# Kernel optimization log

Measured on AMD Instinct MI355X. Metric: run time of the kernel, lower is better.

The kernel has to match this reference:

```python
import jax, jax.numpy as jnp
import numpy as np

N = 20000      # nodes
E = 640000     # edges
HID = 128      # hidden_dim
HEADS = 8
HD = HID // HEADS  # head_dim = 16


def setup_inputs() -> dict:
    key = jax.random.key(0)
    ks = jax.random.split(key, 32)
    s = 1.0 / np.sqrt(HID)
    d = {}
    d["h"] = jax.random.normal(ks[0], (N, HID), jnp.float32)
    d["x"] = jax.random.normal(ks[1], (N, 3), jnp.float32)
    d["src"] = jax.random.randint(ks[2], (E,), 0, N)
    d["dst"] = jax.random.randint(ks[3], (E,), 0, N)
    d["distances"] = jax.random.uniform(ks[4], (E,), jnp.float32)
    d["bpp_edge_bias"] = jax.random.uniform(ks[5], (E,), jnp.float32)
    d["msa_edge_bias"] = jax.random.uniform(ks[6], (E,), jnp.float32)
    d["chem_edge_bias"] = jax.random.uniform(ks[7], (E,), jnp.float32)
    d["relative_offset"] = jax.random.normal(ks[8], (E,), jnp.float32)
    d["chain_break_mask"] = jax.random.uniform(ks[9], (E,), jnp.float32)
    # attention projections (nn.Linear(hidden, hidden): y = x @ W + b)
    for i, nm in enumerate(["Wq", "Wk", "Wv", "Wo"]):
        d[nm] = jax.random.normal(ks[10 + i], (HID, HID), jnp.float32) * s
    for nm in ["bq", "bk", "bv", "bo"]:
        d[nm] = jnp.zeros((HID,), jnp.float32)
    # six Linear(1, heads) edge-bias heads -> weight vector [HEADS] + bias [HEADS]
    for i, nm in enumerate(["dist", "bpp", "msa", "chem", "rel", "chain"]):
        d["w_" + nm] = jax.random.normal(ks[14 + i], (HEADS,), jnp.float32) * 0.1
        d["b_" + nm] = jnp.zeros((HEADS,), jnp.float32)
    # coord_gate: Linear(HID,HID) -> SiLU -> Linear(HID,1) -> Tanh
    d["Wg1"] = jax.random.normal(ks[20], (HID, HID), jnp.float32) * s
    d["bg1"] = jnp.zeros((HID,), jnp.float32)
    d["wg2"] = jax.random.normal(ks[21], (HID, 1), jnp.float32) * s
    d["bg2"] = jnp.zeros((1,), jnp.float32)
    return d


def _edge_bias(feat, w, b):
    # Linear(1, heads) applied to per-edge scalar: [E] -> [E, HEADS]
    return feat[:, None] * w[None, :] + b[None, :]


def reference(h, x, src, dst, distances, bpp_edge_bias, msa_edge_bias,
              chem_edge_bias, relative_offset, chain_break_mask,
              Wq, bq, Wk, bk, Wv, bv, Wo, bo,
              w_dist, b_dist, w_bpp, b_bpp, w_msa, b_msa,
              w_chem, b_chem, w_rel, b_rel, w_chain, b_chain,
              Wg1, bg1, wg2, bg2):
    n = h.shape[0]
    q = (h @ Wq + bq).reshape(n, HEADS, HD)
    k = (h @ Wk + bk).reshape(n, HEADS, HD)
    v = (h @ Wv + bv).reshape(n, HEADS, HD)
    q_src = q[src]   # [E, H, D]
    k_dst = k[dst]
    v_dst = v[dst]
    logits = jnp.einsum('ehd,ehd->eh', q_src, k_dst) / np.sqrt(float(HD))
    logits = (logits
              - _edge_bias(distances * distances, w_dist, b_dist)
              + _edge_bias(bpp_edge_bias, w_bpp, b_bpp)
              + _edge_bias(msa_edge_bias, w_msa, b_msa)
              + _edge_bias(chem_edge_bias, w_chem, b_chem)
              + _edge_bias(relative_offset, w_rel, b_rel)
              + _edge_bias(chain_break_mask, w_chain, b_chain))
    # segment softmax over edges grouped by src node, per head
    m = jax.ops.segment_max(logits, src, num_segments=n)        # [N, H]
    ex = jnp.exp(logits - m[src])                               # [E, H]
    denom = jax.ops.segment_sum(ex, src, num_segments=n)        # [N, H]
    weights = ex / jnp.maximum(denom[src], 1e-9)                # [E, H]
    # weighted scatter-aggregate of values to src nodes
    h_update = jax.ops.segment_sum(v_dst * weights[:, :, None], src,
                                   num_segments=n).reshape(n, HID)
    h_out = h + h_update @ Wo + bo
    # coordinate update
    weights_mean = weights.mean(axis=1)                         # [E]
    disp = jax.ops.segment_sum((x[dst] - x[src]) * weights_mean[:, None],
                               src, num_segments=n)             # [N, 3]
    gate = jnp.tanh(jax.nn.silu(h_out @ Wg1 + bg1) @ wg2 + bg2)  # [N, 1]
    x_out = x + gate * disp
    return h_out, x_out
```

## Files before the change

### kernel.cpp

```cpp
#include <hip/hip_runtime.h>
#include <hip/hip_bf16.h>

#define N_NODES 20000
#define N_EDGES 640000
#define HID 128
#define HEADS 8
#define HD 16
#define NB_SCAN ((N_NODES + 255) / 256)
#define CH 160
#define QKV_BLOCKS 625
#define PREP_BLOCKS 5

typedef __attribute__((ext_vector_type(8))) short bf16x8;
typedef __attribute__((ext_vector_type(4))) float f32x4;

__device__ __forceinline__ float bflo(unsigned u) {
    union { unsigned i; float f; } x; x.i = u << 16; return x.f;
}
__device__ __forceinline__ float bfhi(unsigned u) {
    union { unsigned i; float f; } x; x.i = u & 0xffff0000u; return x.f;
}
__device__ __forceinline__ float bfu(ushort u) {
    union { unsigned i; float f; } x; x.i = ((unsigned)u) << 16; return x.f;
}
__device__ __forceinline__ ushort f2bu(float f) {
    __hip_bfloat16 b = __float2bfloat16(f);
    union { __hip_bfloat16 b; ushort u; } c; c.b = b; return c.u;
}

__global__ __launch_bounds__(256) void hist_prep_kernel(const int* __restrict__ src,
        int* __restrict__ cnt, int* __restrict__ rank,
        const float* __restrict__ Wq, const float* __restrict__ Wk,
        const float* __restrict__ Wv, const float* __restrict__ Wo,
        const float* __restrict__ Wg1, ushort* __restrict__ Wt) {
    if (blockIdx.x < PREP_BLOCKS) {
        const float* srcs[5] = {Wq, Wk, Wv, Wo, Wg1};
        const float* W = srcs[blockIdx.x];
        ushort* out = Wt + (size_t)blockIdx.x * 16384;
        for (int i = threadIdx.x; i < 16384; i += 256) {
            int k = i >> 7, n = i & 127;
            out[n * 128 + k] = f2bu(W[i]);
        }
    } else {
        const int e = (blockIdx.x - PREP_BLOCKS) * 256 + threadIdx.x;
        rank[e] = atomicAdd(&cnt[src[e]], 1);
    }
}

__global__ __launch_bounds__(256) void scan1_kernel(const int* __restrict__ cnt,
        int* __restrict__ startp, int* __restrict__ blockSums, int n) {
    __shared__ int sd[256];
    const int tid = threadIdx.x;
    const int i = blockIdx.x * 256 + tid;
    int xv = (i < n) ? cnt[i] : 0;
    sd[tid] = xv;
    __syncthreads();
#pragma unroll
    for (int off = 1; off < 256; off <<= 1) {
        int tv = (tid >= off) ? sd[tid - off] : 0;
        __syncthreads();
        sd[tid] += tv;
        __syncthreads();
    }
    if (i < n) startp[i] = sd[tid] - xv;
    if (tid == 255) blockSums[blockIdx.x] = sd[255];
}

__global__ __launch_bounds__(128) void scan2_kernel(int* __restrict__ blockSums, int nb) {
    __shared__ int sd[128];
    const int tid = threadIdx.x;
    int xv = (tid < nb) ? blockSums[tid] : 0;
    sd[tid] = xv;
    __syncthreads();
#pragma unroll
    for (int off = 1; off < 128; off <<= 1) {
        int tv = (tid >= off) ? sd[tid - off] : 0;
        __syncthreads();
        sd[tid] += tv;
        __syncthreads();
    }
    if (tid < nb) blockSums[tid] = sd[tid] - xv;
    if (tid == 127) blockSums[nb] = sd[127];
}

__global__ __launch_bounds__(256) void scatter_qkv_kernel(
        const float* __restrict__ h, const ushort* __restrict__ Wt,
        const float* __restrict__ bq, const float* __restrict__ bk,
        const float* __restrict__ bv,
        ushort* __restrict__ qb, ushort* __restrict__ kb, ushort* __restrict__ vb,
        const int* __restrict__ src, const int* __restrict__ dst,
        const float* __restrict__ dist, const float* __restrict__ bpp,
        const float* __restrict__ msa, const float* __restrict__ chem,
        const float* __restrict__ rel, const float* __restrict__ chain,
        const float* __restrict__ w_dist, const float* __restrict__ b_dist,
        const float* __restrict__ w_bpp, const float* __restrict__ b_bpp,
        const float* __restrict__ w_msa, const float* __restrict__ b_msa,
        const float* __restrict__ w_chem, const float* __restrict__ b_chem,
        const float* __restrict__ w_rel, const float* __restrict__ b_rel,
        const float* __restrict__ w_chain, const float* __restrict__ b_chain,
        const int* __restrict__ startp, const int* __restrict__ blockSums,
        const int* __restrict__ rank, const float* __restrict__ x,
        uint4* __restrict__ recs) {
    __shared__ __align__(16) ushort hs[32 * 136];
    const int t = threadIdx.x;
    if (blockIdx.x < QKV_BLOCKS) {
        const int row0 = blockIdx.x * 32;
        for (int i = t; i < 4096; i += 256)
            hs[(i >> 7) * 136 + (i & 127)] = f2bu(h[(size_t)row0 * 128 + i]);
        __syncthreads();
        const int w = t >> 6, lane = t & 63;
        const int rt = w >> 1, half = w & 1;
        const int lrow = lane & 15, lkb = (lane >> 4) * 8;
        bf16x8 a[4];
#pragma unroll
        for (int ks = 0; ks < 4; ++ks)
            a[ks] = *reinterpret_cast<const bf16x8*>(&hs[(rt * 16 + lrow) * 136 + ks * 32 + lkb]);
        __syncthreads();
        const int rloc0 = rt * 16 + (lane >> 4) * 4;
#define DO_MAT(MI, BIAS, OUT) \
        { \
        for (int ctp = 0; ctp < 4; ++ctp) { \
            const int col = (ctp * 2 + half) * 16 + lrow; \
            f32x4 acc = {0.f, 0.f, 0.f, 0.f}; \
            _Pragma("unroll") \
            for (int ks = 0; ks < 4; ++ks) { \
                bf16x8 b = *reinterpret_cast<const bf16x8*>( \
                    &Wt[MI * 16384 + col * 128 + ks * 32 + lkb]); \
                acc = __builtin_amdgcn_mfma_f32_16x16x32_bf16(a[ks], b, acc, 0, 0, 0); \
            } \
            const float bias = BIAS[col]; \
            _Pragma("unroll") \
            for (int r = 0; r < 4; ++r) \
                hs[(rloc0 + r) * 128 + col] = f2bu(acc[r] + bias); \
        } \
        __syncthreads(); \
        { \
            uint4* outp = reinterpret_cast<uint4*>(OUT + (size_t)row0 * 128); \
            const uint4* inp = reinterpret_cast<const uint4*>(hs); \
            outp[t] = inp[t]; \
            outp[t + 256] = inp[t + 256]; \
        } \
        __syncthreads(); \
        }
        DO_MAT(0, bq, qb)
        DO_MAT(1, bk, kb)
        DO_MAT(2, bv, vb)
#undef DO_MAT
    } else {
        const int e = (blockIdx.x - QKV_BLOCKS) * 256 + t;
        const int s = src[e];
        const int pos = startp[s] + blockSums[s >> 8] + rank[e];
        const int dn = dst[e];
        const float d2 = dist[e] * dist[e];
        const float f_bpp = bpp[e], f_msa = msa[e], f_chem = chem[e];
        const float f_rel = rel[e], f_chain = chain[e];
        ushort o16[8];
#pragma unroll
        for (int hq = 0; hq < 8; ++hq) {
            float b = -(d2 * w_dist[hq] + b_dist[hq])
                    + (f_bpp * w_bpp[hq] + b_bpp[hq])
                    + (f_msa * w_msa[hq] + b_msa[hq])
                    + (f_chem * w_chem[hq] + b_chem[hq])
                    + (f_rel * w_rel[hq] + b_rel[hq])
                    + (f_chain * w_chain[hq] + b_chain[hq]);
            o16[hq] = f2bu(b);
        }
        uint4 rec0;
        rec0.x = (unsigned)o16[0] | ((unsigned)o16[1] << 16);
        rec0.y = (unsigned)o16[2] | ((unsigned)o16[3] << 16);
        rec0.z = (unsigned)o16[4] | ((unsigned)o16[5] << 16);
        rec0.w = (unsigned)o16[6] | ((unsigned)o16[7] << 16);
        const float* xp = &x[(size_t)dn * 3];
        uint4 rec1;
        rec1.x = (unsigned)dn;
        rec1.y = __float_as_uint(xp[0]);
        rec1.z = __float_as_uint(xp[1]);
        rec1.w = __float_as_uint(xp[2]);
        recs[(size_t)pos * 2]     = rec0;
        recs[(size_t)pos * 2 + 1] = rec1;
    }
}

__global__ __launch_bounds__(256) void node_kernel(const ushort* __restrict__ qb,
        const ushort* __restrict__ kb, const ushort* __restrict__ vb,
        const uint4* __restrict__ recs, const float* __restrict__ x,
        const int* __restrict__ startp, const int* __restrict__ blockSums,
        ushort* __restrict__ hub, float* __restrict__ disp) {
    __shared__ float qLds[4 * 128];
    __shared__ float xsLds[12];
    __shared__ int   sLds[5];
    __shared__ int   dnLds[CH];
    __shared__ float xLds[CH * 3];
    __shared__ __align__(16) ushort biasLds[CH * 8];
    __shared__ float peLds[CH * 8];
    __shared__ float redN[4][32][9];

    const int t = threadIdx.x;
    const int n0 = blockIdx.x * 4;

    if (t < 64) {
        uint4 qv = reinterpret_cast<const uint4*>(qb + (size_t)n0 * 128)[t];
        const unsigned* qu = reinterpret_cast<const unsigned*>(&qv);
        float4 f0 = make_float4(bflo(qu[0]), bfhi(qu[0]), bflo(qu[1]), bfhi(qu[1]));
        float4 f1 = make_float4(bflo(qu[2]), bfhi(qu[2]), bflo(qu[3]), bfhi(qu[3]));
        *reinterpret_cast<float4*>(&qLds[t * 8])     = f0;
        *reinterpret_cast<float4*>(&qLds[t * 8 + 4]) = f1;
    }
    if (t < 12) xsLds[t] = x[(size_t)n0 * 3 + t];
    if (t < 5) {
        int idx = n0 + t;
        sLds[t] = (idx < N_NODES) ? (startp[idx] + blockSums[idx >> 8]) : N_EDGES;
    }
    __syncthreads();

    const int S0 = sLds[0], S4 = sLds[4];
    const int s1r = sLds[1], s2r = sLds[2], s3r = sLds[3];

    const int eg = t >> 5;
    const int dq = t & 31;
    const int hh = dq >> 2;
    const int jj = dq & 3;
    const int j3 = (jj < 3) ? jj : 0;

    float acc0[4] = {0,0,0,0}, acc1[4] = {0,0,0,0};
    float acc2[4] = {0,0,0,0}, acc3[4] = {0,0,0,0};
    float den0 = 0, den1 = 0, den2 = 0, den3 = 0;
    float adx0 = 0, adx1 = 0, adx2 = 0, adx3 = 0;

    for (int base = S0; base < S4; base += CH) {
        const int en = min(CH, S4 - base);
        __syncthreads();
        if (t < en) {
            const uint4 r0 = recs[(size_t)(base + t) * 2];
            const uint4 r1 = recs[(size_t)(base + t) * 2 + 1];
            *reinterpret_cast<uint4*>(&biasLds[t * 8]) = r0;
            dnLds[t] = (int)r1.x;
            xLds[t * 3 + 0] = __uint_as_float(r1.y);
            xLds[t * 3 + 1] = __uint_as_float(r1.z);
            xLds[t * 3 + 2] = __uint_as_float(r1.w);
        }
        __syncthreads();
        const int np = en * 8;
#define PA_BODY(P) { \
            const int e = (P) >> 3, ha = (P) & 7; \
            const int ge = base + e; \
            const int m = (ge >= s1r) + (ge >= s2r) + (ge >= s3r); \
            const ushort* krow = kb + (size_t)dnLds[e] * 128 + ha * 16; \
            const uint4 ka = *reinterpret_cast<const uint4*>(krow); \
            const uint4 kb4 = *reinterpret_cast<const uint4*>(krow + 8); \
            const float* qrow = &qLds[m * 128 + ha * 16]; \
            const unsigned* kau = reinterpret_cast<const unsigned*>(&ka); \
            const unsigned* kbu = reinterpret_cast<const unsigned*>(&kb4); \
            float s0 = 0.f, s1 = 0.f, s2 = 0.f, s3 = 0.f; \
            _Pragma("unroll") \
            for (int i = 0; i < 4; ++i) { \
                s0 = fmaf(bflo(kau[i]), qrow[2 * i],     s0); \
                s1 = fmaf(bfhi(kau[i]), qrow[2 * i + 1], s1); \
                s2 = fmaf(bflo(kbu[i]), qrow[8 + 2 * i],     s2); \
                s3 = fmaf(bfhi(kbu[i]), qrow[8 + 2 * i + 1], s3); \
            } \
            peLds[P] = __expf(fmaf((s0 + s1) + (s2 + s3), 0.25f, bfu(biasLds[P]))); \
        }
        {
            int p = t;
            for (; p + 256 < np; p += 512) { PA_BODY(p) PA_BODY(p + 256) }
            if (p < np) PA_BODY(p)
        }
#undef PA_BODY
        __syncthreads();
#define PC_BODY(E, ACC, DEN, ADX, XSV) { \
            const float pe = peLds[(E) * 8 + hh]; \
            const ushort4 vv = *reinterpret_cast<const ushort4*>( \
                vb + (size_t)dnLds[E] * 128 + dq * 4); \
            ACC[0] = fmaf(pe, bfu(vv.x), ACC[0]); \
            ACC[1] = fmaf(pe, bfu(vv.y), ACC[1]); \
            ACC[2] = fmaf(pe, bfu(vv.z), ACC[2]); \
            ACC[3] = fmaf(pe, bfu(vv.w), ACC[3]); \
            DEN += pe; \
            ADX = fmaf(pe, xLds[(E) * 3 + j3] - XSV, ADX); \
        }
#define NODE_C(M, ACC, DEN, ADX) { \
            const int lo = max(sLds[M] - base, 0); \
            const int hi = min(sLds[M + 1] - base, en); \
            const float xsv = xsLds[M * 3 + j3]; \
            int e = lo + eg; \
            for (; e + 8 < hi; e += 16) { \
                PC_BODY(e, ACC, DEN, ADX, xsv) \
                PC_BODY(e + 8, ACC, DEN, ADX, xsv) \
            } \
            if (e < hi) PC_BODY(e, ACC, DEN, ADX, xsv) \
        }
        NODE_C(0, acc0, den0, adx0)
        NODE_C(1, acc1, den1, adx1)
        NODE_C(2, acc2, den2, adx2)
        NODE_C(3, acc3, den3, adx3)
#undef NODE_C
#undef PC_BODY
    }

    const int wv = t >> 6, lane = t & 63;
#define RED_M(M, ACC, DEN, ADX) { \
        float r0 = ACC[0], r1 = ACC[1], r2 = ACC[2], r3 = ACC[3]; \
        float rd = DEN, rx = (jj < 3) ? ADX : 0.f; \
        r0 += __shfl_xor(r0, 32); r1 += __shfl_xor(r1, 32); \
        r2 += __shfl_xor(r2, 32); r3 += __shfl_xor(r3, 32); \
        rd += __shfl_xor(rd, 32); rx += __shfl_xor(rx, 32); \
        if (lane < 32) { \
            redN[wv][lane][0] = r0; redN[wv][lane][1] = r1; \
            redN[wv][lane][2] = r2; redN[wv][lane][3] = r3; \
            redN[wv][lane][4] = rd; redN[wv][lane][5] = rx; \
        } \
        __syncthreads(); \
        if (t < 128) { \
            const int dqr = t >> 2, vi = t & 3; \
            float s = redN[0][dqr][vi] + redN[1][dqr][vi] \
                    + redN[2][dqr][vi] + redN[3][dqr][vi]; \
            float d = redN[0][dqr][4] + redN[1][dqr][4] \
                    + redN[2][dqr][4] + redN[3][dqr][4]; \
            hub[(size_t)(n0 + M) * 128 + t] = f2bu(s / fmaxf(d, 1e-9f)); \
        } \
        if (t < 32) { \
            float v = redN[0][t][5] + redN[1][t][5] + redN[2][t][5] + redN[3][t][5]; \
            float d = redN[0][t][4] + redN[1][t][4] + redN[2][t][4] + redN[3][t][4]; \
            float s = v / fmaxf(d, 1e-9f); \
            s += __shfl_xor(s, 4); s += __shfl_xor(s, 8); s += __shfl_xor(s, 16); \
            if (t < 3) disp[(size_t)(n0 + M) * 3 + t] = s * 0.125f; \
        } \
        __syncthreads(); }
    RED_M(0, acc0, den0, adx0)
    RED_M(1, acc1, den1, adx1)
    RED_M(2, acc2, den2, adx2)
    RED_M(3, acc3, den3, adx3)
#undef RED_M
}

__global__ __launch_bounds__(256) void out_kernel(const float* __restrict__ h,
        const float* __restrict__ x, const ushort* __restrict__ hub,
        const ushort* __restrict__ Wt,
        const float* __restrict__ bo, const float* __restrict__ bg1,
        const float* __restrict__ wg2, const float* __restrict__ bg2,
        const float* __restrict__ disp,
        float* __restrict__ hout, float* __restrict__ xout) {
    __shared__ __align__(16) ushort hus[32 * 136];
    __shared__ __align__(16) float hof[32 * 132];
    __shared__ float g1s[32 * 132];
    const int t = threadIdx.x;
    const int row0 = blockIdx.x * 32;
    for (int i8 = t; i8 < 512; i8 += 256) {
        const int row = i8 >> 4, c8 = (i8 & 15) * 8;
        *reinterpret_cast<uint4*>(&hus[row * 136 + c8]) =
            reinterpret_cast<const uint4*>(hub + (size_t)row0 * 128)[i8];
    }
    for (int i4 = t; i4 < 1024; i4 += 256) {
        const int row = i4 >> 5, c4 = (i4 & 31) * 4;
        *reinterpret_cast<float4*>(&hof[row * 132 + c4]) =
            reinterpret_cast<const float4*>(h + (size_t)row0 * 128)[i4];
    }
    __syncthreads();
    const int w = t >> 6, lane = t & 63;
    const int rt = w >> 1, half = w & 1;
    const int lrow = lane & 15, lkb = (lane >> 4) * 8;
    const int rloc = rt * 16 + (lane >> 4) * 4;
    bf16x8 a[4];
#pragma unroll
    for (int ks = 0; ks < 4; ++ks)
        a[ks] = *reinterpret_cast<const bf16x8*>(&hus[(rt * 16 + lrow) * 136 + ks * 32 + lkb]);
    for (int ctp = 0; ctp < 4; ++ctp) {
        const int col = (ctp * 2 + half) * 16 + lrow;
        f32x4 acc = {0.f, 0.f, 0.f, 0.f};
#pragma unroll
        for (int ks = 0; ks < 4; ++ks) {
            bf16x8 b = *reinterpret_cast<const bf16x8*>(&Wt[3 * 16384 + col * 128 + ks * 32 + lkb]);
            acc = __builtin_amdgcn_mfma_f32_16x16x32_bf16(a[ks], b, acc, 0, 0, 0);
        }
        const float bias = bo[col];
#pragma unroll
        for (int r = 0; r < 4; ++r)
            hof[(rloc + r) * 132 + col] += acc[r] + bias;
    }
    __syncthreads();
    for (int i4 = t; i4 < 1024; i4 += 256) {
        const int row = i4 >> 5, c4 = (i4 & 31) * 4;
        *reinterpret_cast<float4*>(hout + (size_t)(row0 + row) * 128 + c4) =
            *reinterpret_cast<const float4*>(&hof[row * 132 + c4]);
    }
    bf16x8 a2[4];
#pragma unroll
    for (int ks = 0; ks < 4; ++ks) {
        const float* fp = &hof[(rt * 16 + lrow) * 132 + ks * 32 + lkb];
        const float4 f0 = *reinterpret_cast<const float4*>(fp);
        const float4 f1 = *reinterpret_cast<const float4*>(fp + 4);
        bf16x8 v;
        v[0] = (short)f2bu(f0.x); v[1] = (short)f2bu(f0.y);
        v[2] = (short)f2bu(f0.z); v[3] = (short)f2bu(f0.w);
        v[4] = (short)f2bu(f1.x); v[5] = (short)f2bu(f1.y);
        v[6] = (short)f2bu(f1.z); v[7] = (short)f2bu(f1.w);
        a2[ks] = v;
    }
    for (int ctp = 0; ctp < 4; ++ctp) {
        const int col = (ctp * 2 + half) * 16 + lrow;
        f32x4 acc = {0.f, 0.f, 0.f, 0.f};
#pragma unroll
        for (int ks = 0; ks < 4; ++ks) {
            bf16x8 b = *reinterpret_cast<const bf16x8*>(&Wt[4 * 16384 + col * 128 + ks * 32 + lkb]);
            acc = __builtin_amdgcn_mfma_f32_16x16x32_bf16(a2[ks], b, acc, 0, 0, 0);
        }
        const float bias = bg1[col];
#pragma unroll
        for (int r = 0; r < 4; ++r) {
            float av = acc[r] + bias;
            g1s[(rloc + r) * 132 + col] = av / (1.f + __expf(-av));
        }
    }
    __syncthreads();
    {
        const int r = t >> 3, j = t & 7;
        float partial = 0.f;
        for (int cc = j; cc < 128; cc += 8) partial += g1s[r * 132 + cc] * wg2[cc];
        partial += __shfl_xor(partial, 1);
        partial += __shfl_xor(partial, 2);
        partial += __shfl_xor(partial, 4);
        const float gate = tanhf(partial + bg2[0]);
        if (j < 3) {
            const int row = row0 + r;
            xout[(size_t)row * 3 + j] = x[(size_t)row * 3 + j] + gate * disp[(size_t)row * 3 + j];
        }
    }
}


extern "C" void kernel_launch(void* const* d_in, const int* in_sizes, int n_in,
                              void* d_out, int out_size, void* d_ws, size_t ws_size,
                              hipStream_t stream) {
    const float* h     = (const float*)d_in[0];
    const float* x     = (const float*)d_in[1];
    const int*   src   = (const int*)d_in[2];
    const int*   dst   = (const int*)d_in[3];
    const float* dist  = (const float*)d_in[4];
    const float* bpp   = (const float*)d_in[5];
    const float* msa   = (const float*)d_in[6];
    const float* chem  = (const float*)d_in[7];
    const float* rel   = (const float*)d_in[8];
    const float* chain = (const float*)d_in[9];
    const float* Wq = (const float*)d_in[10];
    const float* Wk = (const float*)d_in[11];
    const float* Wv = (const float*)d_in[12];
    const float* Wo = (const float*)d_in[13];
    const float* bq = (const float*)d_in[14];
    const float* bk = (const float*)d_in[15];
    const float* bv = (const float*)d_in[16];
    const float* bo = (const float*)d_in[17];
    const float* w_dist = (const float*)d_in[18];  const float* b_dist = (const float*)d_in[19];
    const float* w_bpp  = (const float*)d_in[20];  const float* b_bpp  = (const float*)d_in[21];
    const float* w_msa  = (const float*)d_in[22];  const float* b_msa  = (const float*)d_in[23];
    const float* w_chem = (const float*)d_in[24];  const float* b_chem = (const float*)d_in[25];
    const float* w_rel  = (const float*)d_in[26];  const float* b_rel  = (const float*)d_in[27];
    const float* w_chain= (const float*)d_in[28];  const float* b_chain= (const float*)d_in[29];
    const float* Wg1 = (const float*)d_in[30];
    const float* bg1 = (const float*)d_in[31];
    const float* wg2 = (const float*)d_in[32];
    const float* bg2 = (const float*)d_in[33];

    char* wp = (char*)d_ws;
    const size_t NH2 = (size_t)N_NODES * HID * sizeof(ushort);
    ushort* hub   = (ushort*)wp;               wp += NH2;
    ushort* qb    = (ushort*)wp;               wp += NH2;
    ushort* kb    = (ushort*)wp;               wp += NH2;
    ushort* vb    = (ushort*)wp;               wp += NH2;
    uint4*  recs  = (uint4*)wp;                wp += (size_t)N_EDGES * 32;
    float*  disp  = (float*)wp;                wp += (size_t)N_NODES * 3 * sizeof(float);
    int* rank     = (int*)wp;                  wp += (size_t)N_EDGES * sizeof(int);
    int* startp   = (int*)wp;                  wp += (size_t)N_NODES * sizeof(int);
    int* cnt      = (int*)wp;                  wp += (size_t)N_NODES * sizeof(int);
    int* blockSums= (int*)wp;                  wp += (size_t)(NB_SCAN + 1) * sizeof(int);
    ushort* Wt    = (ushort*)wp;               wp += (size_t)5 * 16384 * sizeof(ushort);

    float* hout = (float*)d_out;
    float* xout = hout + (size_t)N_NODES * HID;

    hipMemsetAsync(cnt, 0, (size_t)N_NODES * sizeof(int), stream);
    hipLaunchKernelGGL(hist_prep_kernel, dim3(N_EDGES / 256 + PREP_BLOCKS), dim3(256), 0, stream,
                       src, cnt, rank, Wq, Wk, Wv, Wo, Wg1, Wt);
    hipLaunchKernelGGL(scan1_kernel, dim3(NB_SCAN), dim3(256), 0, stream,
                       cnt, startp, blockSums, N_NODES);
    hipLaunchKernelGGL(scan2_kernel, dim3(1), dim3(128), 0, stream, blockSums, NB_SCAN);
    hipLaunchKernelGGL(scatter_qkv_kernel, dim3(QKV_BLOCKS + N_EDGES / 256), dim3(256), 0, stream,
                       h, Wt, bq, bk, bv, qb, kb, vb,
                       src, dst, dist, bpp, msa, chem, rel, chain,
                       w_dist, b_dist, w_bpp, b_bpp, w_msa, b_msa,
                       w_chem, b_chem, w_rel, b_rel, w_chain, b_chain,
                       startp, blockSums, rank, x, recs);
    hipLaunchKernelGGL(node_kernel, dim3(N_NODES / 4), dim3(256), 0, stream,
                       qb, kb, vb, recs, x, startp, blockSums, hub, disp);
    hipLaunchKernelGGL(out_kernel, dim3(N_NODES / 32), dim3(256), 0, stream,
                       h, x, hub, Wt, bo, bg1, wg2, bg2, disp, hout, xout);
}
```

Measured before the change: 163.0 us.

## Split edge records into bias and compact meta arrays and store weights as bf16

Measured after the change: 174.1 us. +6.8%, slower.

```diff
diff --git a/kernel.cpp b/kernel.cpp
--- a/kernel.cpp
+++ b/kernel.cpp
@@ -7,7 +7,7 @@
 #define HEADS 8
 #define HD 16
 #define NB_SCAN ((N_NODES + 255) / 256)
-#define CH 160
+#define CH 192
 #define QKV_BLOCKS 625
 #define PREP_BLOCKS 5
 
@@ -100,7 +100,7 @@
         const float* __restrict__ w_chain, const float* __restrict__ b_chain,
         const int* __restrict__ startp, const int* __restrict__ blockSums,
         const int* __restrict__ rank, const float* __restrict__ x,
-        uint4* __restrict__ recs) {
+        uint4* __restrict__ bias16, uint2* __restrict__ meta) {
     __shared__ __align__(16) ushort hs[32 * 136];
     const int t = threadIdx.x;
     if (blockIdx.x < QKV_BLOCKS) {
@@ -165,38 +165,37 @@
                     + (f_chain * w_chain[hq] + b_chain[hq]);
             o16[hq] = f2bu(b);
         }
-        uint4 rec0;
-        rec0.x = (unsigned)o16[0] | ((unsigned)o16[1] << 16);
-        rec0.y = (unsigned)o16[2] | ((unsigned)o16[3] << 16);
-        rec0.z = (unsigned)o16[4] | ((unsigned)o16[5] << 16);
-        rec0.w = (unsigned)o16[6] | ((unsigned)o16[7] << 16);
+        uint4 b4;
+        b4.x = (unsigned)o16[0] | ((unsigned)o16[1] << 16);
+        b4.y = (unsigned)o16[2] | ((unsigned)o16[3] << 16);
+        b4.z = (unsigned)o16[4] | ((unsigned)o16[5] << 16);
+        b4.w = (unsigned)o16[6] | ((unsigned)o16[7] << 16);
         const float* xp = &x[(size_t)dn * 3];
-        uint4 rec1;
-        rec1.x = (unsigned)dn;
-        rec1.y = __float_as_uint(xp[0]);
-        rec1.z = __float_as_uint(xp[1]);
-        rec1.w = __float_as_uint(xp[2]);
-        recs[(size_t)pos * 2]     = rec0;
-        recs[(size_t)pos * 2 + 1] = rec1;
+        uint2 mt;
+        mt.x = (unsigned)f2bu(xp[0]) | ((unsigned)f2bu(xp[1]) << 16);
+        mt.y = (unsigned)f2bu(xp[2]) | ((unsigned)dn << 16);
+        bias16[pos] = b4;
+        meta[pos]   = mt;
     }
 }
 
 __global__ __launch_bounds__(256) void node_kernel(const ushort* __restrict__ qb,
         const ushort* __restrict__ kb, const ushort* __restrict__ vb,
-        const uint4* __restrict__ recs, const float* __restrict__ x,
+        const uint4* __restrict__ bias16, const uint2* __restrict__ meta,
+        const float* __restrict__ x,
         const int* __restrict__ startp, const int* __restrict__ blockSums,
         ushort* __restrict__ hub, float* __restrict__ disp) {
     __shared__ float qLds[4 * 128];
     __shared__ float xsLds[12];
     __shared__ int   sLds[5];
-    __shared__ int   dnLds[CH];
+    __shared__ ushort dnLds[CH];
     __shared__ float xLds[CH * 3];
-    __shared__ __align__(16) ushort biasLds[CH * 8];
-    __shared__ float peLds[CH * 8];
+    __shared__ ushort pbLds[CH * 8];
     __shared__ float redN[4][32][9];
 
     const int t = threadIdx.x;
     const int n0 = blockIdx.x * 4;
+    const ushort* biasU = reinterpret_cast<const ushort*>(bias16);
 
     if (t < 64) {
         uint4 qv = reinterpret_cast<const uint4*>(qb + (size_t)n0 * 128)[t];
@@ -231,13 +230,11 @@
         const int en = min(CH, S4 - base);
         __syncthreads();
         if (t < en) {
-            const uint4 r0 = recs[(size_t)(base + t) * 2];
-            const uint4 r1 = recs[(size_t)(base + t) * 2 + 1];
-            *reinterpret_cast<uint4*>(&biasLds[t * 8]) = r0;
-            dnLds[t] = (int)r1.x;
-            xLds[t * 3 + 0] = __uint_as_float(r1.y);
-            xLds[t * 3 + 1] = __uint_as_float(r1.z);
-            xLds[t * 3 + 2] = __uint_as_float(r1.w);
+            const uint2 mt = meta[base + t];
+            dnLds[t] = (ushort)(mt.y >> 16);
+            xLds[t * 3 + 0] = bfu((ushort)(mt.x & 0xffff));
+            xLds[t * 3 + 1] = bfu((ushort)(mt.x >> 16));
+            xLds[t * 3 + 2] = bfu((ushort)(mt.y & 0xffff));
         }
         __syncthreads();
         const int np = en * 8;
@@ -248,6 +245,7 @@
             const ushort* krow = kb + (size_t)dnLds[e] * 128 + ha * 16; \
             const uint4 ka = *reinterpret_cast<const uint4*>(krow); \
             const uint4 kb4 = *reinterpret_cast<const uint4*>(krow + 8); \
+            const float bias = bfu(biasU[(size_t)base * 8 + (P)]); \
             const float* qrow = &qLds[m * 128 + ha * 16]; \
             const unsigned* kau = reinterpret_cast<const unsigned*>(&ka); \
             const unsigned* kbu = reinterpret_cast<const unsigned*>(&kb4); \
@@ -259,7 +257,7 @@
                 s2 = fmaf(bflo(kbu[i]), qrow[8 + 2 * i],     s2); \
                 s3 = fmaf(bfhi(kbu[i]), qrow[8 + 2 * i + 1], s3); \
             } \
-            peLds[P] = __expf(fmaf((s0 + s1) + (s2 + s3), 0.25f, bfu(biasLds[P]))); \
+            pbLds[P] = f2bu(__expf(fmaf((s0 + s1) + (s2 + s3), 0.25f, bias))); \
         }
         {
             int p = t;
@@ -269,7 +267,7 @@
 #undef PA_BODY
         __syncthreads();
 #define PC_BODY(E, ACC, DEN, ADX, XSV) { \
-            const float pe = peLds[(E) * 8 + hh]; \
+            const float pe = bfu(pbLds[(E) * 8 + hh]); \
             const ushort4 vv = *reinterpret_cast<const ushort4*>( \
                 vb + (size_t)dnLds[E] * 128 + dq * 4); \
             ACC[0] = fmaf(pe, bfu(vv.x), ACC[0]); \
@@ -467,7 +465,8 @@
     ushort* qb    = (ushort*)wp;               wp += NH2;
     ushort* kb    = (ushort*)wp;               wp += NH2;
     ushort* vb    = (ushort*)wp;               wp += NH2;
-    uint4*  recs  = (uint4*)wp;                wp += (size_t)N_EDGES * 32;
+    uint4*  bias16= (uint4*)wp;                wp += (size_t)N_EDGES * 16;
+    uint2*  meta  = (uint2*)wp;                wp += (size_t)N_EDGES * 8;
     float*  disp  = (float*)wp;                wp += (size_t)N_NODES * 3 * sizeof(float);
     int* rank     = (int*)wp;                  wp += (size_t)N_EDGES * sizeof(int);
     int* startp   = (int*)wp;                  wp += (size_t)N_NODES * sizeof(int);
@@ -489,9 +488,9 @@
                        src, dst, dist, bpp, msa, chem, rel, chain,
                        w_dist, b_dist, w_bpp, b_bpp, w_msa, b_msa,
                        w_chem, b_chem, w_rel, b_rel, w_chain, b_chain,
-                       startp, blockSums, rank, x, recs);
+                       startp, blockSums, rank, x, bias16, meta);
     hipLaunchKernelGGL(node_kernel, dim3(N_NODES / 4), dim3(256), 0, stream,
-                       qb, kb, vb, recs, x, startp, blockSums, hub, disp);
+                       qb, kb, vb, bias16, meta, x, startp, blockSums, hub, disp);
     hipLaunchKernelGGL(out_kernel, dim3(N_NODES / 32), dim3(256), 0, stream,
                        h, x, hub, Wt, bo, bg1, wg2, bg2, disp, hout, xout);
 }
```
